# Performance work log

Hardware: AMD Instinct MI355X
Metric: run time of the kernel (lower is better)

## Reference

```python
import math
import jax, jax.numpy as jnp
import numpy as np

H = 4
C_HID = 32

def setup_inputs() -> dict:
    key = jax.random.key(0)
    ks = jax.random.split(key, 8)
    B, N, C = 1, 256, 128
    q_x = jax.random.normal(ks[0], (B, N, N, C), dtype=jnp.float32)
    kv_x = jax.random.normal(ks[1], (B, N, N, C), dtype=jnp.float32)
    tri_bias = jax.random.normal(ks[2], (B, 1, H, N, N), dtype=jnp.float32)
    mask_bias = jnp.zeros((B, N, 1, 1, N), dtype=jnp.float32)
    mask = jnp.ones((B, N, N, N), dtype=jnp.float32)
    s = 1.0 / math.sqrt(C)
    Wq = jax.random.normal(ks[3], (C, H * C_HID), dtype=jnp.float32) * s
    Wk = jax.random.normal(ks[4], (C, H * C_HID), dtype=jnp.float32) * s
    Wv = jax.random.normal(ks[5], (C, H * C_HID), dtype=jnp.float32) * s
    Wg = jax.random.normal(ks[6], (C, H * C_HID), dtype=jnp.float32) * s
    Wo = jax.random.normal(ks[7], (H * C_HID, C), dtype=jnp.float32) * s
    return {"q_x": q_x, "kv_x": kv_x, "tri_bias": tri_bias, "mask_bias": mask_bias,
            "mask": mask, "Wq": Wq, "Wk": Wk, "Wv": Wv, "Wg": Wg, "Wo": Wo}

def reference(q_x, kv_x, tri_bias, mask_bias, mask, Wq, Wk, Wv, Wg, Wo):
    # q_x/kv_x: [B, N, Q, C]; mask is unused in the non-kernel path (mask_bias carries it)
    lead = q_x.shape[:-1]  # [B, N, Q]
    def split_heads(t):  # [..., H*C_HID] -> [..., H, L, C_HID]
        t = t.reshape(t.shape[:-1] + (H, C_HID))
        return jnp.swapaxes(t, -2, -3)
    q = split_heads(q_x @ Wq) / math.sqrt(C_HID)   # [B, N, H, Q, C_hid]
    k = split_heads(kv_x @ Wk)                      # [B, N, H, K, C_hid]
    v = split_heads(kv_x @ Wv)                      # [B, N, H, K, C_hid]
    a = jnp.einsum('bnhqc,bnhkc->bnhqk', q, k)
    a = a + mask_bias + tri_bias                    # biases broadcast over [B, N, H, Q, K]
    a = jax.nn.softmax(a, axis=-1)
    o = jnp.einsum('bnhqk,bnhkc->bnhqc', a, v)      # [B, N, H, Q, C_hid]
    o = jnp.swapaxes(o, -2, -3)                     # [B, N, Q, H, C_hid]
    g = jax.nn.sigmoid(q_x @ Wg).reshape(lead + (H, C_HID))
    o = o * g
    o = o.reshape(lead + (H * C_HID,))
    return o @ Wo                                   # [B, N, Q, C]
```

## Files before the change

### kernel.cpp

```cpp
#include <hip/hip_runtime.h>
#include <hip/hip_bf16.h>

#define NDIM 256
#define QDIM 256
#define CDIM 128
#define HH 4
#define DD 32
#define RROWS (NDIM * QDIM)

__device__ __forceinline__ float bf2f(unsigned short u) {
    unsigned int x = ((unsigned int)u) << 16;
    return __uint_as_float(x);
}
__device__ __forceinline__ unsigned short f2bf(float f) {
    unsigned int x = __float_as_uint(f);
    unsigned int lsb = (x >> 16) & 1u;
    x += 0x7fffu + lsb;
    return (unsigned short)(x >> 16);
}

typedef __bf16 bf16x8v __attribute__((ext_vector_type(8)));
typedef float  f32x4v  __attribute__((ext_vector_type(4)));
union frag_u { uint4 u; bf16x8v v; };

__device__ __forceinline__ bf16x8v cvt8(float4 f0, float4 f1) {
    bf16x8v r;
    r[0] = (__bf16)f0.x; r[1] = (__bf16)f0.y; r[2] = (__bf16)f0.z; r[3] = (__bf16)f0.w;
    r[4] = (__bf16)f1.x; r[5] = (__bf16)f1.y; r[6] = (__bf16)f1.z; r[7] = (__bf16)f1.w;
    return r;
}

__global__ __launch_bounds__(256, 1) void prep_weights(
    const float* __restrict__ Wq, const float* __restrict__ Wk,
    const float* __restrict__ Wv, const float* __restrict__ Wg,
    const float* __restrict__ Wo, unsigned short* __restrict__ wt)
{
    __shared__ unsigned short t[128][136];
    const int p = blockIdx.x;
    const float* __restrict__ W = (p == 0) ? Wq : (p == 1) ? Wk :
                                  (p == 2) ? Wv : (p == 3) ? Wg : Wo;
    const int tid = threadIdx.x;
    for (int idx = tid; idx < 16384; idx += 256) {
        int k = idx >> 7, n = idx & 127;
        t[k][n] = f2bf(W[idx]);
    }
    __syncthreads();
    unsigned short* dst = wt + (size_t)p * 16384;
    for (int idx = tid; idx < 16384; idx += 256) {
        int n = idx >> 7, k = idx & 127;
        dst[idx] = t[k][n];
    }
}

__global__ __launch_bounds__(256, 2) void proj_mfma(
    const float* __restrict__ qx, const float* __restrict__ kvx,
    const unsigned short* __restrict__ wt,
    unsigned short* __restrict__ q_ws, unsigned short* __restrict__ k_ws,
    unsigned short* __restrict__ v_ws, unsigned short* __restrict__ g_ws)
{
    const int tid = threadIdx.x;
    const int pp = blockIdx.y;
    const float* __restrict__ X = pp ? kvx : qx;
    const unsigned short* __restrict__ WtA = wt + (size_t)(pp ? 1 : 0) * 16384;
    const unsigned short* __restrict__ WtB = wt + (size_t)(pp ? 2 : 3) * 16384;

    const int wv   = tid >> 6;
    const int lane = tid & 63;
    const int col  = lane & 15;
    const int quad = lane >> 4;
    const int r0   = blockIdx.x * 128 + wv * 32;

    f32x4v accA[2][8], accB[2][8];
#pragma unroll
    for (int mt = 0; mt < 2; ++mt)
#pragma unroll
        for (int nt = 0; nt < 8; ++nt) {
            accA[mt][nt] = (f32x4v){0.f, 0.f, 0.f, 0.f};
            accB[mt][nt] = (f32x4v){0.f, 0.f, 0.f, 0.f};
        }

#pragma unroll
    for (int kt = 0; kt < 4; ++kt) {
        frag_u a[2];
#pragma unroll
        for (int mt = 0; mt < 2; ++mt) {
            const float* src = X + (size_t)(r0 + mt * 16 + col) * 128 + kt * 32 + quad * 8;
            float4 f0 = *(const float4*)src;
            float4 f1 = *(const float4*)(src + 4);
            a[mt].v = cvt8(f0, f1);
        }
#pragma unroll
        for (int nt = 0; nt < 8; ++nt) {
            frag_u b0, b1;
            b0.u = *(const uint4*)(WtA + (size_t)(nt * 16 + col) * 128 + kt * 32 + quad * 8);
            b1.u = *(const uint4*)(WtB + (size_t)(nt * 16 + col) * 128 + kt * 32 + quad * 8);
            accA[0][nt] = __builtin_amdgcn_mfma_f32_16x16x32_bf16(a[0].v, b0.v, accA[0][nt], 0, 0, 0);
            accA[1][nt] = __builtin_amdgcn_mfma_f32_16x16x32_bf16(a[1].v, b0.v, accA[1][nt], 0, 0, 0);
            accB[0][nt] = __builtin_amdgcn_mfma_f32_16x16x32_bf16(a[0].v, b1.v, accB[0][nt], 0, 0, 0);
            accB[1][nt] = __builtin_amdgcn_mfma_f32_16x16x32_bf16(a[1].v, b1.v, accB[1][nt], 0, 0, 0);
        }
    }

#pragma unroll
    for (int mt = 0; mt < 2; ++mt) {
#pragma unroll
        for (int r = 0; r < 4; ++r) {
            int row = r0 + mt * 16 + quad * 4 + r;
            int n = row >> 8;
            int si = row & 255;
#pragma unroll
            for (int nt = 0; nt < 8; ++nt) {
                int c = nt * 16 + col;
                int h = c >> 5, d = c & 31;
                if (pp == 0) {
                    float qv = accA[mt][nt][r] * 0.17677669529663687f;
                    q_ws[((size_t)(n * HH + h) * QDIM + si) * DD + d] = f2bf(qv);
                    float s = 1.0f / (1.0f + __expf(-accB[mt][nt][r]));
                    g_ws[(size_t)row * 128 + c] = f2bf(s);
                } else {
                    k_ws[((size_t)(n * HH + h) * QDIM + si) * DD + d] = f2bf(accA[mt][nt][r]);
                    v_ws[((size_t)(n * HH + h) * QDIM + si) * DD + d] = f2bf(accB[mt][nt][r]);
                }
            }
        }
    }
}

__global__ __launch_bounds__(256, 3) void attn_kernel(
    const unsigned short* __restrict__ q_ws, const unsigned short* __restrict__ k_ws,
    const unsigned short* __restrict__ v_ws, const unsigned short* __restrict__ g_ws,
    const float* __restrict__ tri, const float* __restrict__ mb,
    unsigned short* __restrict__ o_ws)
{
    __shared__ unsigned short vl[32 * 264];
    __shared__ unsigned short Pl[64 * 264];
    __shared__ float sinv[4][16];

    const int tid = threadIdx.x;
    const int qc = blockIdx.x;
    const int n  = blockIdx.y;
    const int h  = blockIdx.z;
    const size_t base = (size_t)(n * HH + h) * QDIM * DD;

    for (int t = 0; t < 4; ++t) {
        int idx = tid + t * 256;
        int key = idx >> 2;
        int u = idx & 3;
        union { uint4 q; unsigned short s[8]; } raw;
        raw.q = *(const uint4*)(v_ws + base + (size_t)key * DD + u * 8);
#pragma unroll
        for (int j = 0; j < 8; ++j)
            vl[(u * 8 + j) * 264 + key] = raw.s[j];
    }

    const int wv   = tid >> 6;
    const int lane = tid & 63;
    const int col  = lane & 15;
    const int quad = lane >> 4;
    const int qg   = qc * 64 + wv * 16 + col;

    frag_u bq;
    bq.u = *(const uint4*)(q_ws + base + (size_t)qg * DD + quad * 8);

    f32x4v acc[16];
#pragma unroll
    for (int mt = 0; mt < 16; ++mt) {
        int k0 = mt * 16 + quad * 4;
        float4 t4 = *(const float4*)&tri[((size_t)(h * 256 + qg)) * 256 + k0];
        float4 m4 = *(const float4*)&mb[n * 256 + k0];
        f32x4v c;
        c[0] = t4.x + m4.x; c[1] = t4.y + m4.y;
        c[2] = t4.z + m4.z; c[3] = t4.w + m4.w;
        frag_u ak;
        ak.u = *(const uint4*)(k_ws + base + (size_t)(mt * 16 + col) * DD + quad * 8);
        acc[mt] = __builtin_amdgcn_mfma_f32_16x16x32_bf16(ak.v, bq.v, c, 0, 0, 0);
    }

    float mx = -1e30f;
#pragma unroll
    for (int mt = 0; mt < 16; ++mt)
#pragma unroll
        for (int r = 0; r < 4; ++r) mx = fmaxf(mx, acc[mt][r]);
    mx = fmaxf(mx, __shfl_xor(mx, 16));
    mx = fmaxf(mx, __shfl_xor(mx, 32));

    float sum = 0.f;
#pragma unroll
    for (int mt = 0; mt < 16; ++mt)
#pragma unroll
        for (int r = 0; r < 4; ++r) {
            float e = __expf(acc[mt][r] - mx);
            acc[mt][r] = e;
            sum += e;
        }
    sum += __shfl_xor(sum, 16);
    sum += __shfl_xor(sum, 32);
    if (quad == 0) sinv[wv][col] = 1.0f / sum;

#pragma unroll
    for (int mt = 0; mt < 16; ++mt) {
        ushort4 pk;
        pk.x = f2bf(acc[mt][0]); pk.y = f2bf(acc[mt][1]);
        pk.z = f2bf(acc[mt][2]); pk.w = f2bf(acc[mt][3]);
        *(ushort4*)&Pl[(wv * 16 + col) * 264 + mt * 16 + quad * 4] = pk;
    }

    __syncthreads();

    f32x4v o0 = {0.f, 0.f, 0.f, 0.f};
    f32x4v o1 = {0.f, 0.f, 0.f, 0.f};
#pragma unroll
    for (int kc = 0; kc < 8; ++kc) {
        frag_u ap, b0, b1;
        ap.u = *(const uint4*)&Pl[(wv * 16 + col) * 264 + kc * 32 + quad * 8];
        b0.u = *(const uint4*)&vl[(col) * 264 + kc * 32 + quad * 8];
        b1.u = *(const uint4*)&vl[(16 + col) * 264 + kc * 32 + quad * 8];
        o0 = __builtin_amdgcn_mfma_f32_16x16x32_bf16(ap.v, b0.v, o0, 0, 0, 0);
        o1 = __builtin_amdgcn_mfma_f32_16x16x32_bf16(ap.v, b1.v, o1, 0, 0, 0);
    }

#pragma unroll
    for (int r = 0; r < 4; ++r) {
        int qi = quad * 4 + r;
        int qglob = qc * 64 + wv * 16 + qi;
        float iv = sinv[wv][qi];
        size_t ob = ((size_t)(n * 256 + qglob)) * 128 + h * 32;
        float g0 = bf2f(g_ws[ob + col]);
        o_ws[ob + col] = f2bf(o0[r] * iv * g0);
        float g1 = bf2f(g_ws[ob + 16 + col]);
        o_ws[ob + 16 + col] = f2bf(o1[r] * iv * g1);
    }
}

__global__ __launch_bounds__(256, 4) void outproj_mfma(
    const unsigned short* __restrict__ o_ws, const unsigned short* __restrict__ wt,
    float* __restrict__ out)
{
    const int tid = threadIdx.x;
    const unsigned short* __restrict__ Wt = wt + 4 * 16384;

    const int wv   = tid >> 6;
    const int lane = tid & 63;
    const int col  = lane & 15;
    const int quad = lane >> 4;
    const int r0   = blockIdx.x * 128 + wv * 32;

    f32x4v acc[2][8];
#pragma unroll
    for (int mt = 0; mt < 2; ++mt)
#pragma unroll
        for (int nt = 0; nt < 8; ++nt)
            acc[mt][nt] = (f32x4v){0.f, 0.f, 0.f, 0.f};

#pragma unroll
    for (int kt = 0; kt < 4; ++kt) {
        frag_u a[2];
#pragma unroll
        for (int mt = 0; mt < 2; ++mt)
            a[mt].u = *(const uint4*)(o_ws + (size_t)(r0 + mt * 16 + col) * 128 + kt * 32 + quad * 8);
#pragma unroll
        for (int nt = 0; nt < 8; ++nt) {
            frag_u b;
            b.u = *(const uint4*)(Wt + (size_t)(nt * 16 + col) * 128 + kt * 32 + quad * 8);
            acc[0][nt] = __builtin_amdgcn_mfma_f32_16x16x32_bf16(a[0].v, b.v, acc[0][nt], 0, 0, 0);
            acc[1][nt] = __builtin_amdgcn_mfma_f32_16x16x32_bf16(a[1].v, b.v, acc[1][nt], 0, 0, 0);
        }
    }

#pragma unroll
    for (int mt = 0; mt < 2; ++mt)
#pragma unroll
        for (int r = 0; r < 4; ++r) {
            size_t row = r0 + mt * 16 + quad * 4 + r;
#pragma unroll
            for (int nt = 0; nt < 8; ++nt)
                out[row * 128 + nt * 16 + col] = acc[mt][nt][r];
        }
}

extern "C" void kernel_launch(void* const* d_in, const int* in_sizes, int n_in,
                              void* d_out, int out_size, void* d_ws, size_t ws_size,
                              hipStream_t stream) {
    const float* qx  = (const float*)d_in[0];
    const float* kvx = (const float*)d_in[1];
    const float* tri = (const float*)d_in[2];
    const float* mb  = (const float*)d_in[3];
    const float* Wq  = (const float*)d_in[5];
    const float* Wk  = (const float*)d_in[6];
    const float* Wv  = (const float*)d_in[7];
    const float* Wg  = (const float*)d_in[8];
    const float* Wo  = (const float*)d_in[9];
    float* out = (float*)d_out;

    unsigned short* ws = (unsigned short*)d_ws;
    const size_t RC = (size_t)RROWS * 128;
    unsigned short* q_ws = ws;
    unsigned short* k_ws = ws + RC;
    unsigned short* v_ws = ws + 2 * RC;
    unsigned short* g_ws = ws + 3 * RC;
    unsigned short* o_ws = ws + 4 * RC;
    unsigned short* wt   = ws + 5 * RC;

    prep_weights<<<dim3(5), 256, 0, stream>>>(Wq, Wk, Wv, Wg, Wo, wt);
    proj_mfma<<<dim3(RROWS / 128, 2), 256, 0, stream>>>(
        qx, kvx, wt, q_ws, k_ws, v_ws, g_ws);
    attn_kernel<<<dim3(4, NDIM, HH), 256, 0, stream>>>(
        q_ws, k_ws, v_ws, g_ws, tri, mb, o_ws);
    outproj_mfma<<<dim3(RROWS / 128), 256, 0, stream>>>(o_ws, wt, out);
}
```

Before: 275.7 us.

## Fuse attention with output projection and store V transposed from projection

The attention kernel now gives each warp one head and loops over four 16-query strips. Each block writes its gated output for all four heads into shared memory and then performs the Wo output projection in place, which removes the separate outproj kernel and the o_ws round trip through global memory. The projection kernel writes V in transposed layout so that P·V B-fragments load straight from global memory, with no LDS transpose. The bf16 conversion also uses the native cast. The costs are a grid four times smaller with more serial work per warp, and strided scattered stores when writing V transposed.

Result: slower. 371.0 us (+34.6%).

```diff
diff --git a/kernel.cpp b/kernel.cpp
--- a/kernel.cpp
+++ b/kernel.cpp
@@ -13,10 +13,9 @@
     return __uint_as_float(x);
 }
 __device__ __forceinline__ unsigned short f2bf(float f) {
-    unsigned int x = __float_as_uint(f);
-    unsigned int lsb = (x >> 16) & 1u;
-    x += 0x7fffu + lsb;
-    return (unsigned short)(x >> 16);
+    union { __bf16 b; unsigned short u; } cv;
+    cv.b = (__bf16)f;
+    return cv.u;
 }
 
 typedef __bf16 bf16x8v __attribute__((ext_vector_type(8)));
@@ -56,7 +55,7 @@
     const float* __restrict__ qx, const float* __restrict__ kvx,
     const unsigned short* __restrict__ wt,
     unsigned short* __restrict__ q_ws, unsigned short* __restrict__ k_ws,
-    unsigned short* __restrict__ v_ws, unsigned short* __restrict__ g_ws)
+    unsigned short* __restrict__ vt_ws, unsigned short* __restrict__ g_ws)
 {
     const int tid = threadIdx.x;
     const int pp = blockIdx.y;
@@ -119,163 +118,133 @@
                     g_ws[(size_t)row * 128 + c] = f2bf(s);
                 } else {
                     k_ws[((size_t)(n * HH + h) * QDIM + si) * DD + d] = f2bf(accA[mt][nt][r]);
-                    v_ws[((size_t)(n * HH + h) * QDIM + si) * DD + d] = f2bf(accB[mt][nt][r]);
+                    vt_ws[((size_t)(n * HH + h) * DD + d) * QDIM + si] = f2bf(accB[mt][nt][r]);
                 }
             }
         }
     }
 }
 
-__global__ __launch_bounds__(256, 3) void attn_kernel(
+__global__ __launch_bounds__(256, 3) void attn_out(
     const unsigned short* __restrict__ q_ws, const unsigned short* __restrict__ k_ws,
-    const unsigned short* __restrict__ v_ws, const unsigned short* __restrict__ g_ws,
+    const unsigned short* __restrict__ vt_ws, const unsigned short* __restrict__ g_ws,
     const float* __restrict__ tri, const float* __restrict__ mb,
-    unsigned short* __restrict__ o_ws)
+    const unsigned short* __restrict__ wt, float* __restrict__ out)
 {
-    __shared__ unsigned short vl[32 * 264];
-    __shared__ unsigned short Pl[64 * 264];
-    __shared__ float sinv[4][16];
+    __shared__ unsigned short Pl[4][16 * 264];
+    __shared__ unsigned short Ol[64 * 136];
 
     const int tid = threadIdx.x;
     const int qc = blockIdx.x;
     const int n  = blockIdx.y;
-    const int h  = blockIdx.z;
-    const size_t base = (size_t)(n * HH + h) * QDIM * DD;
-
-    for (int t = 0; t < 4; ++t) {
-        int idx = tid + t * 256;
-        int key = idx >> 2;
-        int u = idx & 3;
-        union { uint4 q; unsigned short s[8]; } raw;
-        raw.q = *(const uint4*)(v_ws + base + (size_t)key * DD + u * 8);
-#pragma unroll
-        for (int j = 0; j < 8; ++j)
-            vl[(u * 8 + j) * 264 + key] = raw.s[j];
-    }
-
     const int wv   = tid >> 6;
+    const int h    = wv;
     const int lane = tid & 63;
     const int col  = lane & 15;
     const int quad = lane >> 4;
-    const int qg   = qc * 64 + wv * 16 + col;
-
-    frag_u bq;
-    bq.u = *(const uint4*)(q_ws + base + (size_t)qg * DD + quad * 8);
-
-    f32x4v acc[16];
-#pragma unroll
-    for (int mt = 0; mt < 16; ++mt) {
-        int k0 = mt * 16 + quad * 4;
-        float4 t4 = *(const float4*)&tri[((size_t)(h * 256 + qg)) * 256 + k0];
-        float4 m4 = *(const float4*)&mb[n * 256 + k0];
-        f32x4v c;
-        c[0] = t4.x + m4.x; c[1] = t4.y + m4.y;
-        c[2] = t4.z + m4.z; c[3] = t4.w + m4.w;
-        frag_u ak;
-        ak.u = *(const uint4*)(k_ws + base + (size_t)(mt * 16 + col) * DD + quad * 8);
-        acc[mt] = __builtin_amdgcn_mfma_f32_16x16x32_bf16(ak.v, bq.v, c, 0, 0, 0);
-    }
-
-    float mx = -1e30f;
-#pragma unroll
-    for (int mt = 0; mt < 16; ++mt)
-#pragma unroll
-        for (int r = 0; r < 4; ++r) mx = fmaxf(mx, acc[mt][r]);
-    mx = fmaxf(mx, __shfl_xor(mx, 16));
-    mx = fmaxf(mx, __shfl_xor(mx, 32));
-
-    float sum = 0.f;
-#pragma unroll
-    for (int mt = 0; mt < 16; ++mt)
+    const size_t base  = (size_t)(n * HH + h) * QDIM * DD;
+    const size_t vbase = (size_t)(n * HH + h) * DD * QDIM;
+    unsigned short* Pw = &Pl[wv][0];
+
+    for (int st = 0; st < 4; ++st) {
+        const int qg = qc * 64 + st * 16 + col;
+
+        frag_u bq;
+        bq.u = *(const uint4*)(q_ws + base + (size_t)qg * DD + quad * 8);
+
+        f32x4v acc[16];
+#pragma unroll
+        for (int mt = 0; mt < 16; ++mt) {
+            int k0 = mt * 16 + quad * 4;
+            float4 t4 = *(const float4*)&tri[((size_t)(h * 256 + qg)) * 256 + k0];
+            float4 m4 = *(const float4*)&mb[n * 256 + k0];
+            f32x4v c;
+            c[0] = t4.x + m4.x; c[1] = t4.y + m4.y;
+            c[2] = t4.z + m4.z; c[3] = t4.w + m4.w;
+            frag_u ak;
+            ak.u = *(const uint4*)(k_ws + base + (size_t)(mt * 16 + col) * DD + quad * 8);
+            acc[mt] = __builtin_amdgcn_mfma_f32_16x16x32_bf16(ak.v, bq.v, c, 0, 0, 0);
+        }
+
+        float mx = -1e30f;
+#pragma unroll
+        for (int mt = 0; mt < 16; ++mt)
+#pragma unroll
+            for (int r = 0; r < 4; ++r) mx = fmaxf(mx, acc[mt][r]);
+        mx = fmaxf(mx, __shfl_xor(mx, 16));
+        mx = fmaxf(mx, __shfl_xor(mx, 32));
+
+        float sum = 0.f;
+#pragma unroll
+        for (int mt = 0; mt < 16; ++mt)
+#pragma unroll
+            for (int r = 0; r < 4; ++r) {
+                float e = __expf(acc[mt][r] - mx);
+                acc[mt][r] = e;
+                sum += e;
+            }
+        sum += __shfl_xor(sum, 16);
+        sum += __shfl_xor(sum, 32);
+        float inv = 1.0f / sum;
+
+#pragma unroll
+        for (int mt = 0; mt < 16; ++mt) {
+            ushort4 pk;
+            pk.x = f2bf(acc[mt][0]); pk.y = f2bf(acc[mt][1]);
+            pk.z = f2bf(acc[mt][2]); pk.w = f2bf(acc[mt][3]);
+            *(ushort4*)&Pw[col * 264 + mt * 16 + quad * 4] = pk;
+        }
+
+        f32x4v o0 = {0.f, 0.f, 0.f, 0.f};
+        f32x4v o1 = {0.f, 0.f, 0.f, 0.f};
+#pragma unroll
+        for (int kc = 0; kc < 8; ++kc) {
+            frag_u ap, b0, b1;
+            ap.u = *(const uint4*)&Pw[col * 264 + kc * 32 + quad * 8];
+            b0.u = *(const uint4*)(vt_ws + vbase + (size_t)col * QDIM + kc * 32 + quad * 8);
+            b1.u = *(const uint4*)(vt_ws + vbase + (size_t)(16 + col) * QDIM + kc * 32 + quad * 8);
+            o0 = __builtin_amdgcn_mfma_f32_16x16x32_bf16(ap.v, b0.v, o0, 0, 0, 0);
+            o1 = __builtin_amdgcn_mfma_f32_16x16x32_bf16(ap.v, b1.v, o1, 0, 0, 0);
+        }
+
 #pragma unroll
         for (int r = 0; r < 4; ++r) {
-            float e = __expf(acc[mt][r] - mx);
-            acc[mt][r] = e;
-            sum += e;
-        }
-    sum += __shfl_xor(sum, 16);
-    sum += __shfl_xor(sum, 32);
-    if (quad == 0) sinv[wv][col] = 1.0f / sum;
-
-#pragma unroll
-    for (int mt = 0; mt < 16; ++mt) {
-        ushort4 pk;
-        pk.x = f2bf(acc[mt][0]); pk.y = f2bf(acc[mt][1]);
-        pk.z = f2bf(acc[mt][2]); pk.w = f2bf(acc[mt][3]);
-        *(ushort4*)&Pl[(wv * 16 + col) * 264 + mt * 16 + quad * 4] = pk;
+            int qi = st * 16 + quad * 4 + r;
+            float iv = __shfl(inv, quad * 4 + r);
+            size_t grow = ((size_t)(n * 256 + qc * 64 + qi)) * 128 + h * 32;
+            float g0 = bf2f(g_ws[grow + col]);
+            Ol[qi * 136 + h * 32 + col] = f2bf(o0[r] * iv * g0);
+            float g1 = bf2f(g_ws[grow + 16 + col]);
+            Ol[qi * 136 + h * 32 + 16 + col] = f2bf(o1[r] * iv * g1);
+        }
     }
 
     __syncthreads();
 
-    f32x4v o0 = {0.f, 0.f, 0.f, 0.f};
-    f32x4v o1 = {0.f, 0.f, 0.f, 0.f};
-#pragma unroll
-    for (int kc = 0; kc < 8; ++kc) {
-        frag_u ap, b0, b1;
-        ap.u = *(const uint4*)&Pl[(wv * 16 + col) * 264 + kc * 32 + quad * 8];
-        b0.u = *(const uint4*)&vl[(col) * 264 + kc * 32 + quad * 8];
-        b1.u = *(const uint4*)&vl[(16 + col) * 264 + kc * 32 + quad * 8];
-        o0 = __builtin_amdgcn_mfma_f32_16x16x32_bf16(ap.v, b0.v, o0, 0, 0, 0);
-        o1 = __builtin_amdgcn_mfma_f32_16x16x32_bf16(ap.v, b1.v, o1, 0, 0, 0);
-    }
-
-#pragma unroll
-    for (int r = 0; r < 4; ++r) {
-        int qi = quad * 4 + r;
-        int qglob = qc * 64 + wv * 16 + qi;
-        float iv = sinv[wv][qi];
-        size_t ob = ((size_t)(n * 256 + qglob)) * 128 + h * 32;
-        float g0 = bf2f(g_ws[ob + col]);
-        o_ws[ob + col] = f2bf(o0[r] * iv * g0);
-        float g1 = bf2f(g_ws[ob + 16 + col]);
-        o_ws[ob + 16 + col] = f2bf(o1[r] * iv * g1);
-    }
-}
-
-__global__ __launch_bounds__(256, 4) void outproj_mfma(
-    const unsigned short* __restrict__ o_ws, const unsigned short* __restrict__ wt,
-    float* __restrict__ out)
-{
-    const int tid = threadIdx.x;
     const unsigned short* __restrict__ Wt = wt + 4 * 16384;
-
-    const int wv   = tid >> 6;
-    const int lane = tid & 63;
-    const int col  = lane & 15;
-    const int quad = lane >> 4;
-    const int r0   = blockIdx.x * 128 + wv * 32;
-
-    f32x4v acc[2][8];
-#pragma unroll
-    for (int mt = 0; mt < 2; ++mt)
-#pragma unroll
-        for (int nt = 0; nt < 8; ++nt)
-            acc[mt][nt] = (f32x4v){0.f, 0.f, 0.f, 0.f};
+    f32x4v acc2[8];
+#pragma unroll
+    for (int nt = 0; nt < 8; ++nt) acc2[nt] = (f32x4v){0.f, 0.f, 0.f, 0.f};
 
 #pragma unroll
     for (int kt = 0; kt < 4; ++kt) {
-        frag_u a[2];
-#pragma unroll
-        for (int mt = 0; mt < 2; ++mt)
-            a[mt].u = *(const uint4*)(o_ws + (size_t)(r0 + mt * 16 + col) * 128 + kt * 32 + quad * 8);
+        frag_u a;
+        a.u = *(const uint4*)&Ol[(wv * 16 + col) * 136 + kt * 32 + quad * 8];
 #pragma unroll
         for (int nt = 0; nt < 8; ++nt) {
             frag_u b;
             b.u = *(const uint4*)(Wt + (size_t)(nt * 16 + col) * 128 + kt * 32 + quad * 8);
-            acc[0][nt] = __builtin_amdgcn_mfma_f32_16x16x32_bf16(a[0].v, b.v, acc[0][nt], 0, 0, 0);
-            acc[1][nt] = __builtin_amdgcn_mfma_f32_16x16x32_bf16(a[1].v, b.v, acc[1][nt], 0, 0, 0);
-        }
-    }
-
-#pragma unroll
-    for (int mt = 0; mt < 2; ++mt)
-#pragma unroll
-        for (int r = 0; r < 4; ++r) {
-            size_t row = r0 + mt * 16 + quad * 4 + r;
-#pragma unroll
-            for (int nt = 0; nt < 8; ++nt)
-                out[row * 128 + nt * 16 + col] = acc[mt][nt][r];
-        }
+            acc2[nt] = __builtin_amdgcn_mfma_f32_16x16x32_bf16(a.v, b.v, acc2[nt], 0, 0, 0);
+        }
+    }
+
+#pragma unroll
+    for (int r = 0; r < 4; ++r) {
+        size_t row = (size_t)(n * 256 + qc * 64 + wv * 16 + quad * 4 + r);
+#pragma unroll
+        for (int nt = 0; nt < 8; ++nt)
+            out[row * 128 + nt * 16 + col] = acc2[nt][r];
+    }
 }
 
 extern "C" void kernel_launch(void* const* d_in, const int* in_sizes, int n_in,
@@ -294,17 +263,15 @@
 
     unsigned short* ws = (unsigned short*)d_ws;
     const size_t RC = (size_t)RROWS * 128;
-    unsigned short* q_ws = ws;
-    unsigned short* k_ws = ws + RC;
-    unsigned short* v_ws = ws + 2 * RC;
-    unsigned short* g_ws = ws + 3 * RC;
-    unsigned short* o_ws = ws + 4 * RC;
-    unsigned short* wt   = ws + 5 * RC;
+    unsigned short* q_ws  = ws;
+    unsigned short* k_ws  = ws + RC;
+    unsigned short* vt_ws = ws + 2 * RC;
+    unsigned short* g_ws  = ws + 3 * RC;
+    unsigned short* wt    = ws + 4 * RC;
 
     prep_weights<<<dim3(5), 256, 0, stream>>>(Wq, Wk, Wv, Wg, Wo, wt);
     proj_mfma<<<dim3(RROWS / 128, 2), 256, 0, stream>>>(
-        qx, kvx, wt, q_ws, k_ws, v_ws, g_ws);
-    attn_kernel<<<dim3(4, NDIM, HH), 256, 0, stream>>>(
-        q_ws, k_ws, v_ws, g_ws, tri, mb, o_ws);
-    outproj_mfma<<<dim3(RROWS / 128), 256, 0, stream>>>(o_ws, wt, out);
-}
+        qx, kvx, wt, q_ws, k_ws, vt_ws, g_ws);
+    attn_out<<<dim3(4, NDIM), 256, 0, stream>>>(
+        q_ws, k_ws, vt_ws, g_ws, tri, mb, wt, out);
+}
```

## Pre-transpose V in projection, use per-wave P tiles, remap attention grid for XCD locality

Applied to the files above, without the earlier changes.

The projection kernel now writes V transposed (d-major), so the attention kernel can stage it into shared memory with vector copies instead of scalar scatter stores. Shared memory shrinks: P is held in per-wave 16x72 chunks written and consumed in steps, and the softmax normalizer travels by lane shuffle instead of through shared memory. That drops the block-wide barrier before the PV MFMAs and lets launch bounds rise from 3 to 5 blocks. The grid is flattened and remapped so that blocks sharing an n land on the same XCD, for L2 reuse of K/V. f2bf now uses the compiler's bf16 conversion. The projection's transposed V store is strided and may write less efficiently.

After: 296.8 us. 1.08x slower.

```diff
diff --git a/kernel.cpp b/kernel.cpp
--- a/kernel.cpp
+++ b/kernel.cpp
@@ -13,10 +13,9 @@
     return __uint_as_float(x);
 }
 __device__ __forceinline__ unsigned short f2bf(float f) {
-    unsigned int x = __float_as_uint(f);
-    unsigned int lsb = (x >> 16) & 1u;
-    x += 0x7fffu + lsb;
-    return (unsigned short)(x >> 16);
+    union { __bf16 b; unsigned short u; } cv;
+    cv.b = (__bf16)f;
+    return cv.u;
 }
 
 typedef __bf16 bf16x8v __attribute__((ext_vector_type(8)));
@@ -56,7 +55,7 @@
     const float* __restrict__ qx, const float* __restrict__ kvx,
     const unsigned short* __restrict__ wt,
     unsigned short* __restrict__ q_ws, unsigned short* __restrict__ k_ws,
-    unsigned short* __restrict__ v_ws, unsigned short* __restrict__ g_ws)
+    unsigned short* __restrict__ vt_ws, unsigned short* __restrict__ g_ws)
 {
     const int tid = threadIdx.x;
     const int pp = blockIdx.y;
@@ -119,39 +118,43 @@
                     g_ws[(size_t)row * 128 + c] = f2bf(s);
                 } else {
                     k_ws[((size_t)(n * HH + h) * QDIM + si) * DD + d] = f2bf(accA[mt][nt][r]);
-                    v_ws[((size_t)(n * HH + h) * QDIM + si) * DD + d] = f2bf(accB[mt][nt][r]);
+                    vt_ws[((size_t)(n * HH + h) * DD + d) * QDIM + si] = f2bf(accB[mt][nt][r]);
                 }
             }
         }
     }
 }
 
-__global__ __launch_bounds__(256, 3) void attn_kernel(
+__global__ __launch_bounds__(256, 5) void attn_kernel(
     const unsigned short* __restrict__ q_ws, const unsigned short* __restrict__ k_ws,
-    const unsigned short* __restrict__ v_ws, const unsigned short* __restrict__ g_ws,
+    const unsigned short* __restrict__ vt_ws, const unsigned short* __restrict__ g_ws,
     const float* __restrict__ tri, const float* __restrict__ mb,
     unsigned short* __restrict__ o_ws)
 {
     __shared__ unsigned short vl[32 * 264];
-    __shared__ unsigned short Pl[64 * 264];
-    __shared__ float sinv[4][16];
+    __shared__ unsigned short Pl[4][16 * 72];
 
     const int tid = threadIdx.x;
-    const int qc = blockIdx.x;
-    const int n  = blockIdx.y;
-    const int h  = blockIdx.z;
-    const size_t base = (size_t)(n * HH + h) * QDIM * DD;
-
-    for (int t = 0; t < 4; ++t) {
-        int idx = tid + t * 256;
-        int key = idx >> 2;
-        int u = idx & 3;
-        union { uint4 q; unsigned short s[8]; } raw;
-        raw.q = *(const uint4*)(v_ws + base + (size_t)key * DD + u * 8);
-#pragma unroll
-        for (int j = 0; j < 8; ++j)
-            vl[(u * 8 + j) * 264 + key] = raw.s[j];
-    }
+    const int b   = blockIdx.x;
+    const int xcd = b & 7;
+    const int t   = b >> 3;
+    const int u   = t & 15;
+    const int n   = (t >> 4) * 8 + xcd;
+    const int qc  = u >> 2;
+    const int h   = u & 3;
+
+    const size_t base  = (size_t)(n * HH + h) * QDIM * DD;
+    const size_t vbase = (size_t)(n * HH + h) * DD * QDIM;
+
+#pragma unroll
+    for (int i = 0; i < 4; ++i) {
+        int idx = tid + i * 256;
+        int d = idx >> 5;
+        int g = idx & 31;
+        uint4 raw = *(const uint4*)(vt_ws + vbase + (size_t)d * QDIM + g * 8);
+        *(uint4*)&vl[d * 264 + g * 8] = raw;
+    }
+    __syncthreads();
 
     const int wv   = tid >> 6;
     const int lane = tid & 63;
@@ -195,35 +198,38 @@
         }
     sum += __shfl_xor(sum, 16);
     sum += __shfl_xor(sum, 32);
-    if (quad == 0) sinv[wv][col] = 1.0f / sum;
-
-#pragma unroll
-    for (int mt = 0; mt < 16; ++mt) {
-        ushort4 pk;
-        pk.x = f2bf(acc[mt][0]); pk.y = f2bf(acc[mt][1]);
-        pk.z = f2bf(acc[mt][2]); pk.w = f2bf(acc[mt][3]);
-        *(ushort4*)&Pl[(wv * 16 + col) * 264 + mt * 16 + quad * 4] = pk;
-    }
-
-    __syncthreads();
-
+    float inv = 1.0f / sum;
+
+    unsigned short* Pw = &Pl[wv][0];
     f32x4v o0 = {0.f, 0.f, 0.f, 0.f};
     f32x4v o1 = {0.f, 0.f, 0.f, 0.f};
 #pragma unroll
-    for (int kc = 0; kc < 8; ++kc) {
-        frag_u ap, b0, b1;
-        ap.u = *(const uint4*)&Pl[(wv * 16 + col) * 264 + kc * 32 + quad * 8];
-        b0.u = *(const uint4*)&vl[(col) * 264 + kc * 32 + quad * 8];
-        b1.u = *(const uint4*)&vl[(16 + col) * 264 + kc * 32 + quad * 8];
-        o0 = __builtin_amdgcn_mfma_f32_16x16x32_bf16(ap.v, b0.v, o0, 0, 0, 0);
-        o1 = __builtin_amdgcn_mfma_f32_16x16x32_bf16(ap.v, b1.v, o1, 0, 0, 0);
+    for (int cc = 0; cc < 4; ++cc) {
+#pragma unroll
+        for (int j = 0; j < 4; ++j) {
+            int mt = cc * 4 + j;
+            ushort4 pk;
+            pk.x = f2bf(acc[mt][0]); pk.y = f2bf(acc[mt][1]);
+            pk.z = f2bf(acc[mt][2]); pk.w = f2bf(acc[mt][3]);
+            *(ushort4*)&Pw[col * 72 + j * 16 + quad * 4] = pk;
+        }
+#pragma unroll
+        for (int j2 = 0; j2 < 2; ++j2) {
+            int kc = cc * 2 + j2;
+            frag_u ap, b0, b1;
+            ap.u = *(const uint4*)&Pw[col * 72 + j2 * 32 + quad * 8];
+            b0.u = *(const uint4*)&vl[col * 264 + kc * 32 + quad * 8];
+            b1.u = *(const uint4*)&vl[(16 + col) * 264 + kc * 32 + quad * 8];
+            o0 = __builtin_amdgcn_mfma_f32_16x16x32_bf16(ap.v, b0.v, o0, 0, 0, 0);
+            o1 = __builtin_amdgcn_mfma_f32_16x16x32_bf16(ap.v, b1.v, o1, 0, 0, 0);
+        }
     }
 
 #pragma unroll
     for (int r = 0; r < 4; ++r) {
         int qi = quad * 4 + r;
         int qglob = qc * 64 + wv * 16 + qi;
-        float iv = sinv[wv][qi];
+        float iv = __shfl(inv, qi);
         size_t ob = ((size_t)(n * 256 + qglob)) * 128 + h * 32;
         float g0 = bf2f(g_ws[ob + col]);
         o_ws[ob + col] = f2bf(o0[r] * iv * g0);
@@ -294,17 +300,17 @@
 
     unsigned short* ws = (unsigned short*)d_ws;
     const size_t RC = (size_t)RROWS * 128;
-    unsigned short* q_ws = ws;
-    unsigned short* k_ws = ws + RC;
-    unsigned short* v_ws = ws + 2 * RC;
-    unsigned short* g_ws = ws + 3 * RC;
-    unsigned short* o_ws = ws + 4 * RC;
-    unsigned short* wt   = ws + 5 * RC;
+    unsigned short* q_ws  = ws;
+    unsigned short* k_ws  = ws + RC;
+    unsigned short* vt_ws = ws + 2 * RC;
+    unsigned short* g_ws  = ws + 3 * RC;
+    unsigned short* o_ws  = ws + 4 * RC;
+    unsigned short* wt    = ws + 5 * RC;
 
     prep_weights<<<dim3(5), 256, 0, stream>>>(Wq, Wk, Wv, Wg, Wo, wt);
     proj_mfma<<<dim3(RROWS / 128, 2), 256, 0, stream>>>(
-        qx, kvx, wt, q_ws, k_ws, v_ws, g_ws);
-    attn_kernel<<<dim3(4, NDIM, HH), 256, 0, stream>>>(
-        q_ws, k_ws, v_ws, g_ws, tri, mb, o_ws);
+        qx, kvx, wt, q_ws, k_ws, vt_ws, g_ws);
+    attn_kernel<<<dim3(4 * NDIM * HH), 256, 0, stream>>>(
+        q_ws, k_ws, vt_ws, g_ws, tri, mb, o_ws);
     outproj_mfma<<<dim3(RROWS / 128), 256, 0, stream>>>(o_ws, wt, out);
 }
```
